# Kernel optimization log

Hardware: AMD Instinct MI355X
Metric: run time of the kernel (lower is better)

## Reference

```python
import jax, jax.numpy as jnp
import numpy as np

HID = 768
INNER = 1536   # hidden_size * expand_factor
NSTATE = 16
KCONV = 4
EPS = 1e-5


def _layernorm(x, w, b):
    mu = jnp.mean(x, axis=-1, keepdims=True)
    var = jnp.mean(jnp.square(x - mu), axis=-1, keepdims=True)
    return (x - mu) * jax.lax.rsqrt(var + EPS) * w + b


def setup_inputs() -> dict:
    key = jax.random.key(0)
    ks = jax.random.split(key, 8)
    B, S = 2, 2048
    s_in = 1.0 / np.sqrt(HID).astype(np.float32)
    s_inner = 1.0 / np.sqrt(INNER).astype(np.float32)
    s_k = 1.0 / np.sqrt(KCONV).astype(np.float32)
    return {
        "x": jax.random.normal(ks[0], (B, S, HID), jnp.float32),
        "norm_w": jnp.ones((HID,), jnp.float32),
        "norm_b": jnp.zeros((HID,), jnp.float32),
        "W_in": jax.random.normal(ks[1], (HID, 2 * INNER), jnp.float32) * s_in,
        "conv_w": jax.random.normal(ks[2], (INNER, 1, KCONV), jnp.float32) * s_k,  # OIH depthwise
        "W_xproj": jax.random.normal(ks[3], (INNER, 2 * NSTATE + INNER), jnp.float32) * s_inner,
        "A_log": jax.random.normal(ks[4], (NSTATE,), jnp.float32),
        "D": jnp.ones((INNER,), jnp.float32),
        "W_ssm_out": jax.random.normal(ks[5], (INNER, INNER), jnp.float32) * s_inner,
        "W_out": jax.random.normal(ks[6], (INNER, HID), jnp.float32) * s_inner,
    }


def _selective_ssm(u, W_xproj, A_log, D, W_ssm_out):
    # u: (B, S, INNER)
    proj = u @ W_xproj                                   # (B,S,2N+INNER)
    Bm = proj[..., :NSTATE]                              # (B,S,N)
    Cm = proj[..., NSTATE:2 * NSTATE]                    # (B,S,N)
    delta = jax.nn.softplus(proj[..., 2 * NSTATE:])      # (B,S,INNER)
    A = -jnp.exp(A_log)                                  # (N,)

    def step(h, inp):
        d_t, b_t, c_t, u_t = inp                          # (B,INNER),(B,N),(B,N),(B,INNER)
        dA = jnp.exp(d_t[:, None, :] * A[None, :, None])  # (B,N,INNER)
        h = dA * h + (d_t * u_t)[:, None, :] * b_t[:, :, None]
        y = jnp.einsum('bnh,bn->bh', h, c_t)
        return h, y

    B_, S_, _ = u.shape
    h0 = jnp.zeros((B_, NSTATE, INNER), u.dtype)
    xs = (jnp.moveaxis(delta, 1, 0), jnp.moveaxis(Bm, 1, 0),
          jnp.moveaxis(Cm, 1, 0), jnp.moveaxis(u, 1, 0))
    _, ys = jax.lax.scan(step, h0, xs)                   # (S,B,INNER)
    y = jnp.moveaxis(ys, 0, 1) + D * u
    return y @ W_ssm_out


def reference(x, norm_w, norm_b, W_in, conv_w, W_xproj, A_log, D, W_ssm_out, W_out):
    residual = x
    xn = _layernorm(x, norm_w, norm_b)
    xp = xn @ W_in                                       # (B,S,2*INNER)
    u, gate = jnp.split(xp, 2, axis=-1)
    # causal depthwise conv1d (torch pads k-1 both sides then truncates -> left pad k-1)
    uc = jax.lax.conv_general_dilated(
        jnp.swapaxes(u, 1, 2), conv_w, window_strides=(1,),
        padding=[(KCONV - 1, 0)], dimension_numbers=('NCH', 'OIH', 'NCH'),
        feature_group_count=INNER)
    u = jax.nn.silu(jnp.swapaxes(uc, 1, 2))              # (B,S,INNER)
    y = _selective_ssm(u, W_xproj, A_log, D, W_ssm_out)
    y = y * jax.nn.silu(gate)
    out = y @ W_out + residual                           # dropout is identity in eval
    return out
```

## Files before the change

### kernel.cpp

```cpp
#include <hip/hip_runtime.h>
#include <cstdint>
#include <cmath>

#define HID 768
#define INNER 1536
#define NST 16
#define SEQ 2048
#define BATCH 2
#define MTOK 4096
#define CHUNK 32
#define NCHUNK 64
#define LOG2E 1.44269504088896f

typedef unsigned short u16;
typedef __bf16 bf16x8 __attribute__((ext_vector_type(8)));
typedef float f32x4 __attribute__((ext_vector_type(4)));

__device__ __forceinline__ u16 f2b(float f) {
  union { float f; unsigned u; } a; a.f = f;
  unsigned r = a.u + 0x7FFFu + ((a.u >> 16) & 1u);
  return (u16)(r >> 16);
}
__device__ __forceinline__ float b2f(u16 h) {
  union { unsigned u; float f; } a; a.u = ((unsigned)h) << 16; return a.f;
}

__device__ __forceinline__ void gl2lds16(const u16* g, u16* l) {
  __builtin_amdgcn_global_load_lds(
      (const __attribute__((address_space(1))) void*)g,
      (__attribute__((address_space(3))) void*)l, 16, 0, 0);
}

__global__ __launch_bounds__(256)
void ln_kernel(const float* __restrict__ x, const float* __restrict__ w,
               const float* __restrict__ b, u16* __restrict__ xn) {
  const long row = blockIdx.x;
  const float* xr = x + row * HID;
  const int t = threadIdx.x;
  float v0 = xr[t], v1 = xr[t + 256], v2 = xr[t + 512];
  float s1 = v0 + v1 + v2;
  float s2 = v0 * v0 + v1 * v1 + v2 * v2;
#pragma unroll
  for (int o = 32; o > 0; o >>= 1) { s1 += __shfl_down(s1, o); s2 += __shfl_down(s2, o); }
  __shared__ float r1[4], r2[4];
  if ((t & 63) == 0) { r1[t >> 6] = s1; r2[t >> 6] = s2; }
  __syncthreads();
  s1 = r1[0] + r1[1] + r1[2] + r1[3];
  s2 = r2[0] + r2[1] + r2[2] + r2[3];
  const float mu = s1 * (1.f / HID);
  float var = s2 * (1.f / HID) - mu * mu;
  const float rs = rsqrtf(var + 1e-5f);
  xn[row * HID + t]       = f2b((v0 - mu) * rs * w[t]       + b[t]);
  xn[row * HID + t + 256] = f2b((v1 - mu) * rs * w[t + 256] + b[t + 256]);
  xn[row * HID + t + 512] = f2b((v2 - mu) * rs * w[t + 512] + b[t + 512]);
}

__global__ __launch_bounds__(256)
void transpose_cvt(const float* __restrict__ W, u16* __restrict__ Wt,
                   int K, int N, int Npad) {
  __shared__ float tb[32][33];
  const int tx = threadIdx.x, ty = threadIdx.y;
  const int n0 = blockIdx.x * 32, k0 = blockIdx.y * 32;
#pragma unroll
  for (int r = 0; r < 4; ++r) {
    int kk = k0 + ty + r * 8;
    int nn = n0 + tx;
    tb[ty + r * 8][tx] = (nn < N) ? W[(long)kk * N + nn] : 0.f;
  }
  __syncthreads();
#pragma unroll
  for (int r = 0; r < 4; ++r) {
    int nn = n0 + ty + r * 8;
    int kk = k0 + tx;
    Wt[(long)nn * K + kk] = f2b(tb[tx][ty + r * 8]);
  }
}

template <int BM, int BN, int NBX, int EPI>
__global__ __launch_bounds__(256)
void gemm_bt(const u16* __restrict__ A, const u16* __restrict__ Bt,
             float* __restrict__ O0, float* __restrict__ O1, u16* __restrict__ O2,
             const float* __restrict__ Ef, const u16* __restrict__ Eb,
             int K, int Nstore) {
  constexpr int NBY = 4096 / BM;
  constexpr int PER = NBY / 8;
  constexpr int WTM = BM / 2;
  constexpr int WTN = BN / 2;
  constexpr int FI = WTM / 16;
  constexpr int FJ = WTN / 16;
  __shared__ u16 As[BM * 32];
  __shared__ u16 Bs[BN * 32];
  const int u = blockIdx.x;
  const int xcd = u & 7;
  const int s = u >> 3;
  const int bmt = xcd * PER + s / NBX;
  const int bnt = s % NBX;
  const long bm = (long)bmt * BM;
  const long bn = (long)bnt * BN;

  const int tid = threadIdx.x;
  const int lane = tid & 63;
  const int wave = tid >> 6;
  const int wm = wave >> 1, wn = wave & 1;
  const int l16 = lane & 15, l4 = lane >> 4;

  f32x4 acc[FI][FJ] = {};

  const int r0 = tid >> 2;
  const int kg = (tid & 3) * 8;

  for (int k0 = 0; k0 < K; k0 += 32) {
#pragma unroll
    for (int q = 0; q < BM / 64; ++q)
      gl2lds16(A + (bm + r0 + q * 64) * K + kg + k0, As + ((q * 256 + tid) * 8));
#pragma unroll
    for (int q = 0; q < BN / 64; ++q)
      gl2lds16(Bt + (bn + r0 + q * 64) * K + kg + k0, Bs + ((q * 256 + tid) * 8));
    __syncthreads();
    bf16x8 af[FI], bfr[FJ];
#pragma unroll
    for (int i = 0; i < FI; ++i)
      af[i] = *(const bf16x8*)&As[(wm * WTM + i * 16 + l16) * 32 + l4 * 8];
#pragma unroll
    for (int j = 0; j < FJ; ++j)
      bfr[j] = *(const bf16x8*)&Bs[(wn * WTN + j * 16 + l16) * 32 + l4 * 8];
#pragma unroll
    for (int i = 0; i < FI; ++i)
#pragma unroll
      for (int j = 0; j < FJ; ++j)
        acc[i][j] = __builtin_amdgcn_mfma_f32_16x16x32_bf16(af[i], bfr[j], acc[i][j], 0, 0, 0);
    __syncthreads();
  }

#pragma unroll
  for (int i = 0; i < FI; ++i) {
    const long rr = bm + wm * WTM + i * 16 + l4 * 4;
#pragma unroll
    for (int j = 0; j < FJ; ++j) {
      const int cc = (int)bn + wn * WTN + j * 16 + l16;
#pragma unroll
      for (int r = 0; r < 4; ++r) {
        const long row = rr + r;
        const float v = acc[i][j][r];
        if (EPI == 0) {
          if (cc < 1536) O0[row * 1536 + cc] = v;
          else {
            float sv = v / (1.f + __expf(-v));
            O2[row * 1536 + (cc - 1536)] = f2b(sv);
          }
        } else if (EPI == 1) {
          if (cc < 16) O0[row * 16 + cc] = v;
          else if (cc < 32) O1[row * 16 + (cc - 16)] = v;
          else if (cc < Nstore) {
            float sp = (v > 20.f) ? v : log1pf(__expf(v));
            O2[row * 1536 + (cc - 32)] = f2b(sp);
          }
        } else if (EPI == 2) {
          float g = b2f(Eb[row * 1536 + cc]);
          O2[row * 1536 + cc] = f2b(v * g);
        } else {
          O0[row * 768 + cc] = v + Ef[row * 768 + cc];
        }
      }
    }
  }
}

__global__ __launch_bounds__(256)
void conv_silu(const float* __restrict__ xpu, const float* __restrict__ cw,
               u16* __restrict__ ub) {
  const int c = blockIdx.x * 256 + threadIdx.x;
  const long m = blockIdx.y;
  const int t = (int)(m & (SEQ - 1));
  const float w0 = cw[c * 4 + 0], w1 = cw[c * 4 + 1], w2 = cw[c * 4 + 2], w3 = cw[c * 4 + 3];
  float acc = w3 * xpu[m * 1536 + c];
  if (t >= 1) acc += w2 * xpu[(m - 1) * 1536 + c];
  if (t >= 2) acc += w1 * xpu[(m - 2) * 1536 + c];
  if (t >= 3) acc += w0 * xpu[(m - 3) * 1536 + c];
  const float s = acc / (1.f + __expf(-acc));
  ub[m * 1536 + c] = f2b(s);
}

__global__ __launch_bounds__(256)
void scan_phaseA(const u16* __restrict__ dlt, const u16* __restrict__ ub,
                 const float* __restrict__ Bm, const float* __restrict__ A_log,
                 float* __restrict__ P, float* __restrict__ Q) {
  const int tid = threadIdx.x;
  const int cl = tid >> 2;
  const int sg = tid & 3;
  const int c = blockIdx.x * 64 + cl;
  const int b = blockIdx.y;
  const int ch = blockIdx.z;
  float a2[4];
#pragma unroll
  for (int j = 0; j < 4; ++j) a2[j] = -__expf(A_log[sg * 4 + j]) * LOG2E;
  float h[4] = {0.f, 0.f, 0.f, 0.f};
  float sumd = 0.f;
  const long base = (long)b * SEQ + (long)ch * CHUNK;
  for (int t = 0; t < CHUNK; ++t) {
    const long m = base + t;
    const float d = b2f(dlt[m * 1536 + c]);
    const float du = d * b2f(ub[m * 1536 + c]);
    sumd += d;
    const f32x4 Bv = *(const f32x4*)&Bm[m * 16 + sg * 4];
#pragma unroll
    for (int j = 0; j < 4; ++j) {
      const float e = exp2f(a2[j] * d);
      h[j] = e * h[j] + du * Bv[j];
    }
  }
  const long sb = (((long)b * NCHUNK + ch) * NST + sg * 4) * 1536 + c;
#pragma unroll
  for (int j = 0; j < 4; ++j) {
    Q[sb + (long)j * 1536] = h[j];
    P[sb + (long)j * 1536] = exp2f(a2[j] * sumd);
  }
}

__global__ __launch_bounds__(256)
void scan_phaseB(float* __restrict__ P, const float* __restrict__ Q) {
  const long g = (long)blockIdx.x * 256 + threadIdx.x;
  const int c = (int)(g % 1536);
  const int n = (int)((g / 1536) % NST);
  const int b = (int)(g / (1536 * NST));
  float h = 0.f;
  for (int ch = 0; ch < NCHUNK; ++ch) {
    const long idx = (((long)b * NCHUNK + ch) * NST + n) * 1536 + c;
    const float p = P[idx];
    const float q = Q[idx];
    P[idx] = h;
    h = p * h + q;
  }
}

__global__ __launch_bounds__(256)
void scan_phaseC(const u16* __restrict__ dlt, const u16* __restrict__ ub,
                 const float* __restrict__ Bm, const float* __restrict__ Cm,
                 const float* __restrict__ A_log, const float* __restrict__ Dv,
                 const float* __restrict__ hs, u16* __restrict__ ys) {
  const int tid = threadIdx.x;
  const int cl = tid >> 2;
  const int sg = tid & 3;
  const int c = blockIdx.x * 64 + cl;
  const int b = blockIdx.y;
  const int ch = blockIdx.z;
  float a2[4];
#pragma unroll
  for (int j = 0; j < 4; ++j) a2[j] = -__expf(A_log[sg * 4 + j]) * LOG2E;
  float h[4];
  const long sb = (((long)b * NCHUNK + ch) * NST + sg * 4) * 1536 + c;
#pragma unroll
  for (int j = 0; j < 4; ++j) h[j] = hs[sb + (long)j * 1536];
  const float Dc = Dv[c];
  const long base = (long)b * SEQ + (long)ch * CHUNK;
  for (int t = 0; t < CHUNK; ++t) {
    const long m = base + t;
    const float d = b2f(dlt[m * 1536 + c]);
    const float uu = b2f(ub[m * 1536 + c]);
    const float du = d * uu;
    const f32x4 Bv = *(const f32x4*)&Bm[m * 16 + sg * 4];
    const f32x4 Cv = *(const f32x4*)&Cm[m * 16 + sg * 4];
    float y = (sg == 0) ? Dc * uu : 0.f;
#pragma unroll
    for (int j = 0; j < 4; ++j) {
      const float e = exp2f(a2[j] * d);
      h[j] = e * h[j] + du * Bv[j];
      y += h[j] * Cv[j];
    }
    y += __shfl_xor(y, 1);
    y += __shfl_xor(y, 2);
    if (sg == 0) ys[m * 1536 + c] = f2b(y);
  }
}

extern "C" void kernel_launch(void* const* d_in, const int* in_sizes, int n_in,
                              void* d_out, int out_size, void* d_ws, size_t ws_size,
                              hipStream_t stream) {
  const float* x     = (const float*)d_in[0];
  const float* nw    = (const float*)d_in[1];
  const float* nb    = (const float*)d_in[2];
  const float* W_in  = (const float*)d_in[3];
  const float* cw    = (const float*)d_in[4];
  const float* W_xp  = (const float*)d_in[5];
  const float* A_log = (const float*)d_in[6];
  const float* Dv    = (const float*)d_in[7];
  const float* W_so  = (const float*)d_in[8];
  const float* W_out = (const float*)d_in[9];
  float* out = (float*)d_out;

  char* w = (char*)d_ws;
  auto alloc = [&](size_t bytes) {
    char* p = w;
    w += (bytes + 255) & ~(size_t)255;
    return p;
  };
  u16*   xn    = (u16*)  alloc((size_t)MTOK * HID * 2);
  u16*   WtIn  = (u16*)  alloc((size_t)3072 * 768 * 2);
  float* xpu   = (float*)alloc((size_t)MTOK * 1536 * 4);
  u16*   sg    = (u16*)  alloc((size_t)MTOK * 1536 * 2);
  u16*   ub    = (u16*)  alloc((size_t)MTOK * 1536 * 2);
  u16*   WtXp  = (u16*)  alloc((size_t)1664 * 1536 * 2);
  float* Bmv   = (float*)alloc((size_t)MTOK * 16 * 4);
  float* Cmv   = (float*)alloc((size_t)MTOK * 16 * 4);
  u16*   dlt   = (u16*)  alloc((size_t)MTOK * 1536 * 2);
  float* P     = (float*)alloc((size_t)BATCH * NCHUNK * NST * 1536 * 4);
  float* Q     = (float*)alloc((size_t)BATCH * NCHUNK * NST * 1536 * 4);
  u16*   ys    = (u16*)  alloc((size_t)MTOK * 1536 * 2);
  u16*   WtSo  = (u16*)  alloc((size_t)1536 * 1536 * 2);
  u16*   zb    = (u16*)  alloc((size_t)MTOK * 1536 * 2);
  u16*   WtOut = (u16*)  alloc((size_t)768 * 1536 * 2);

  ln_kernel<<<MTOK, 256, 0, stream>>>(x, nw, nb, xn);
  transpose_cvt<<<dim3(3072 / 32, 768 / 32), dim3(32, 8), 0, stream>>>(W_in, WtIn, 768, 3072, 3072);
  transpose_cvt<<<dim3(1664 / 32, 1536 / 32), dim3(32, 8), 0, stream>>>(W_xp, WtXp, 1536, 1568, 1664);
  transpose_cvt<<<dim3(1536 / 32, 1536 / 32), dim3(32, 8), 0, stream>>>(W_so, WtSo, 1536, 1536, 1536);
  transpose_cvt<<<dim3(768 / 32, 1536 / 32), dim3(32, 8), 0, stream>>>(W_out, WtOut, 1536, 768, 768);

  gemm_bt<128, 128, 24, 0><<<768, 256, 0, stream>>>(xn, WtIn, xpu, nullptr, sg, nullptr, nullptr, 768, 3072);
  conv_silu<<<dim3(6, MTOK), 256, 0, stream>>>(xpu, cw, ub);
  gemm_bt<128, 64, 26, 1><<<832, 256, 0, stream>>>(ub, WtXp, Bmv, Cmv, dlt, nullptr, nullptr, 1536, 1568);
  scan_phaseA<<<dim3(24, 2, NCHUNK), 256, 0, stream>>>(dlt, ub, Bmv, A_log, P, Q);
  scan_phaseB<<<192, 256, 0, stream>>>(P, Q);
  scan_phaseC<<<dim3(24, 2, NCHUNK), 256, 0, stream>>>(dlt, ub, Bmv, Cmv, A_log, Dv, P, ys);
  gemm_bt<128, 64, 24, 2><<<768, 256, 0, stream>>>(ys, WtSo, nullptr, nullptr, zb, nullptr, sg, 1536, 1536);
  gemm_bt<64, 64, 12, 3><<<768, 256, 0, stream>>>(zb, WtOut, out, nullptr, nullptr, x, nullptr, 1536, 768);
}
```

Measured before the change: 399.1 us.

## Pack GEMM operands into MFMA fragment order and load directly to registers

Activations and weights are written in a pre-tiled layout that matches the 16x16x32 MFMA fragment order, so each lane's 8-element fragment is one contiguous 16-byte load. The GEMM drops LDS staging and both barriers per k-step and instead double-buffers fragments straight from global memory into registers. Producer kernels (layernorm, conv, scan, gating epilogue) now write the packed layout, and conv writes an extra packed copy. The trade-off is that operand tiles are no longer shared through LDS, so reuse now depends on L2, and the scattered packed-layout stores in the producers may coalesce less well.

```diff
diff --git a/kernel.cpp b/kernel.cpp
--- a/kernel.cpp
+++ b/kernel.cpp
@@ -15,6 +15,7 @@
 typedef unsigned short u16;
 typedef __bf16 bf16x8 __attribute__((ext_vector_type(8)));
 typedef float f32x4 __attribute__((ext_vector_type(4)));
+typedef u16 u16x8 __attribute__((ext_vector_type(8)));
 
 __device__ __forceinline__ u16 f2b(float f) {
   union { float f; unsigned u; } a; a.f = f;
@@ -25,15 +26,13 @@
   union { unsigned u; float f; } a; a.u = ((unsigned)h) << 16; return a.f;
 }
 
-__device__ __forceinline__ void gl2lds16(const u16* g, u16* l) {
-  __builtin_amdgcn_global_load_lds(
-      (const __attribute__((address_space(1))) void*)g,
-      (__attribute__((address_space(3))) void*)l, 16, 0, 0);
+__device__ __forceinline__ long pidx(long m, int k, int KS) {
+  return (((m >> 4) * (long)KS + (k >> 5)) * 64 + ((k >> 3) & 3) * 16 + (m & 15)) * 8 + (k & 7);
 }
 
 __global__ __launch_bounds__(256)
 void ln_kernel(const float* __restrict__ x, const float* __restrict__ w,
-               const float* __restrict__ b, u16* __restrict__ xn) {
+               const float* __restrict__ b, u16* __restrict__ xnp) {
   const long row = blockIdx.x;
   const float* xr = x + row * HID;
   const int t = threadIdx.x;
@@ -50,94 +49,96 @@
   const float mu = s1 * (1.f / HID);
   float var = s2 * (1.f / HID) - mu * mu;
   const float rs = rsqrtf(var + 1e-5f);
-  xn[row * HID + t]       = f2b((v0 - mu) * rs * w[t]       + b[t]);
-  xn[row * HID + t + 256] = f2b((v1 - mu) * rs * w[t + 256] + b[t + 256]);
-  xn[row * HID + t + 512] = f2b((v2 - mu) * rs * w[t + 512] + b[t + 512]);
-}
-
-__global__ __launch_bounds__(256)
-void transpose_cvt(const float* __restrict__ W, u16* __restrict__ Wt,
-                   int K, int N, int Npad) {
-  __shared__ float tb[32][33];
-  const int tx = threadIdx.x, ty = threadIdx.y;
-  const int n0 = blockIdx.x * 32, k0 = blockIdx.y * 32;
-#pragma unroll
-  for (int r = 0; r < 4; ++r) {
-    int kk = k0 + ty + r * 8;
-    int nn = n0 + tx;
-    tb[ty + r * 8][tx] = (nn < N) ? W[(long)kk * N + nn] : 0.f;
+  xnp[pidx(row, t,       24)] = f2b((v0 - mu) * rs * w[t]       + b[t]);
+  xnp[pidx(row, t + 256, 24)] = f2b((v1 - mu) * rs * w[t + 256] + b[t + 256]);
+  xnp[pidx(row, t + 512, 24)] = f2b((v2 - mu) * rs * w[t + 512] + b[t + 512]);
+}
+
+__global__ __launch_bounds__(256)
+void pack_w(const float* __restrict__ W, u16* __restrict__ Bp, int K, int N) {
+  __shared__ float tb[32][65];
+  const int t = threadIdx.x;
+  const int n0 = blockIdx.x * 64;
+  const int ks = blockIdx.y;
+  const int k0 = ks * 32;
+  const int KS = K >> 5;
+  {
+    const int col = t & 63, row0 = t >> 6;
+    const int nn = n0 + col;
+#pragma unroll
+    for (int rr = 0; rr < 8; ++rr) {
+      const int kk = k0 + row0 + rr * 4;
+      tb[row0 + rr * 4][col] = (nn < N) ? W[(long)kk * N + nn] : 0.f;
+    }
   }
   __syncthreads();
-#pragma unroll
-  for (int r = 0; r < 4; ++r) {
-    int nn = n0 + ty + r * 8;
-    int kk = k0 + tx;
-    Wt[(long)nn * K + kk] = f2b(tb[tx][ty + r * 8]);
-  }
-}
-
-template <int BM, int BN, int NBX, int EPI>
-__global__ __launch_bounds__(256)
-void gemm_bt(const u16* __restrict__ A, const u16* __restrict__ Bt,
+  const int ntl = t >> 6, l4 = (t >> 4) & 3, l16 = t & 15;
+  const int nl = ntl * 16 + l16;
+  u16x8 outv;
+#pragma unroll
+  for (int wdx = 0; wdx < 8; ++wdx) outv[wdx] = f2b(tb[l4 * 8 + wdx][nl]);
+  const long tile = (n0 >> 4) + ntl;
+  *(u16x8*)&Bp[(tile * KS + ks) * 512 + (l4 * 16 + l16) * 8] = outv;
+}
+
+template <int FI, int FJ, int NBLK, int EPI>
+__global__ __launch_bounds__(256)
+void gemm_pk(const u16* __restrict__ Ap, const u16* __restrict__ Bp,
              float* __restrict__ O0, float* __restrict__ O1, u16* __restrict__ O2,
              const float* __restrict__ Ef, const u16* __restrict__ Eb,
              int K, int Nstore) {
-  constexpr int NBY = 4096 / BM;
-  constexpr int PER = NBY / 8;
-  constexpr int WTM = BM / 2;
-  constexpr int WTN = BN / 2;
-  constexpr int FI = WTM / 16;
-  constexpr int FJ = WTN / 16;
-  __shared__ u16 As[BM * 32];
-  __shared__ u16 Bs[BN * 32];
+  constexpr int WM = 256 / FI;
+  constexpr int PERX = WM / 16;
+  const int KS = K >> 5;
   const int u = blockIdx.x;
+  const int wave = threadIdx.x >> 6;
+  const int lane = threadIdx.x & 63;
   const int xcd = u & 7;
   const int s = u >> 3;
-  const int bmt = xcd * PER + s / NBX;
-  const int bnt = s % NBX;
-  const long bm = (long)bmt * BM;
-  const long bn = (long)bnt * BN;
-
-  const int tid = threadIdx.x;
-  const int lane = tid & 63;
-  const int wave = tid >> 6;
-  const int wm = wave >> 1, wn = wave & 1;
+  const int wmrow = (xcd * PERX + s / NBLK) * 2 + (wave >> 1);
+  const int wn = (s % NBLK) * 2 + (wave & 1);
+
+  const u16* a0 = Ap + ((long)(wmrow * FI) * KS * 64 + lane) * 8;
+  const u16* b0 = Bp + ((long)(wn * FJ) * KS * 64 + lane) * 8;
+
+  f32x4 acc[FI][FJ] = {};
+  bf16x8 afA[FI], bfA[FJ], afB[FI], bfB[FJ];
+
+#pragma unroll
+  for (int i = 0; i < FI; ++i) afA[i] = *(const bf16x8*)(a0 + (long)i * KS * 512);
+#pragma unroll
+  for (int j = 0; j < FJ; ++j) bfA[j] = *(const bf16x8*)(b0 + (long)j * KS * 512);
+
+  for (int ks = 0; ks < KS; ks += 2) {
+#pragma unroll
+    for (int i = 0; i < FI; ++i) afB[i] = *(const bf16x8*)(a0 + ((long)i * KS + ks + 1) * 512);
+#pragma unroll
+    for (int j = 0; j < FJ; ++j) bfB[j] = *(const bf16x8*)(b0 + ((long)j * KS + ks + 1) * 512);
+#pragma unroll
+    for (int i = 0; i < FI; ++i)
+#pragma unroll
+      for (int j = 0; j < FJ; ++j)
+        acc[i][j] = __builtin_amdgcn_mfma_f32_16x16x32_bf16(afA[i], bfA[j], acc[i][j], 0, 0, 0);
+    if (ks + 2 < KS) {
+#pragma unroll
+      for (int i = 0; i < FI; ++i) afA[i] = *(const bf16x8*)(a0 + ((long)i * KS + ks + 2) * 512);
+#pragma unroll
+      for (int j = 0; j < FJ; ++j) bfA[j] = *(const bf16x8*)(b0 + ((long)j * KS + ks + 2) * 512);
+    }
+#pragma unroll
+    for (int i = 0; i < FI; ++i)
+#pragma unroll
+      for (int j = 0; j < FJ; ++j)
+        acc[i][j] = __builtin_amdgcn_mfma_f32_16x16x32_bf16(afB[i], bfB[j], acc[i][j], 0, 0, 0);
+  }
+
   const int l16 = lane & 15, l4 = lane >> 4;
-
-  f32x4 acc[FI][FJ] = {};
-
-  const int r0 = tid >> 2;
-  const int kg = (tid & 3) * 8;
-
-  for (int k0 = 0; k0 < K; k0 += 32) {
-#pragma unroll
-    for (int q = 0; q < BM / 64; ++q)
-      gl2lds16(A + (bm + r0 + q * 64) * K + kg + k0, As + ((q * 256 + tid) * 8));
-#pragma unroll
-    for (int q = 0; q < BN / 64; ++q)
-      gl2lds16(Bt + (bn + r0 + q * 64) * K + kg + k0, Bs + ((q * 256 + tid) * 8));
-    __syncthreads();
-    bf16x8 af[FI], bfr[FJ];
-#pragma unroll
-    for (int i = 0; i < FI; ++i)
-      af[i] = *(const bf16x8*)&As[(wm * WTM + i * 16 + l16) * 32 + l4 * 8];
-#pragma unroll
-    for (int j = 0; j < FJ; ++j)
-      bfr[j] = *(const bf16x8*)&Bs[(wn * WTN + j * 16 + l16) * 32 + l4 * 8];
-#pragma unroll
-    for (int i = 0; i < FI; ++i)
-#pragma unroll
-      for (int j = 0; j < FJ; ++j)
-        acc[i][j] = __builtin_amdgcn_mfma_f32_16x16x32_bf16(af[i], bfr[j], acc[i][j], 0, 0, 0);
-    __syncthreads();
-  }
-
 #pragma unroll
   for (int i = 0; i < FI; ++i) {
-    const long rr = bm + wm * WTM + i * 16 + l4 * 4;
+    const long rr = (long)(wmrow * FI + i) * 16 + l4 * 4;
 #pragma unroll
     for (int j = 0; j < FJ; ++j) {
-      const int cc = (int)bn + wn * WTN + j * 16 + l16;
+      const int cc = (wn * FJ + j) * 16 + l16;
 #pragma unroll
       for (int r = 0; r < 4; ++r) {
         const long row = rr + r;
@@ -157,7 +158,7 @@
           }
         } else if (EPI == 2) {
           float g = b2f(Eb[row * 1536 + cc]);
-          O2[row * 1536 + cc] = f2b(v * g);
+          O2[pidx(row, cc, 48)] = f2b(v * g);
         } else {
           O0[row * 768 + cc] = v + Ef[row * 768 + cc];
         }
@@ -168,7 +169,7 @@
 
 __global__ __launch_bounds__(256)
 void conv_silu(const float* __restrict__ xpu, const float* __restrict__ cw,
-               u16* __restrict__ ub) {
+               u16* __restrict__ ub, u16* __restrict__ ubp) {
   const int c = blockIdx.x * 256 + threadIdx.x;
   const long m = blockIdx.y;
   const int t = (int)(m & (SEQ - 1));
@@ -178,7 +179,9 @@
   if (t >= 2) acc += w1 * xpu[(m - 2) * 1536 + c];
   if (t >= 3) acc += w0 * xpu[(m - 3) * 1536 + c];
   const float s = acc / (1.f + __expf(-acc));
-  ub[m * 1536 + c] = f2b(s);
+  const u16 sb = f2b(s);
+  ub[m * 1536 + c] = sb;
+  ubp[pidx(m, c, 48)] = sb;
 }
 
 __global__ __launch_bounds__(256)
@@ -237,7 +240,7 @@
 void scan_phaseC(const u16* __restrict__ dlt, const u16* __restrict__ ub,
                  const float* __restrict__ Bm, const float* __restrict__ Cm,
                  const float* __restrict__ A_log, const float* __restrict__ Dv,
-                 const float* __restrict__ hs, u16* __restrict__ ys) {
+                 const float* __restrict__ hs, u16* __restrict__ ysp) {
   const int tid = threadIdx.x;
   const int cl = tid >> 2;
   const int sg = tid & 3;
@@ -269,7 +272,7 @@
     }
     y += __shfl_xor(y, 1);
     y += __shfl_xor(y, 2);
-    if (sg == 0) ys[m * 1536 + c] = f2b(y);
+    if (sg == 0) ysp[pidx(m, c, 48)] = f2b(y);
   }
 }
 
@@ -294,34 +297,35 @@
     w += (bytes + 255) & ~(size_t)255;
     return p;
   };
-  u16*   xn    = (u16*)  alloc((size_t)MTOK * HID * 2);
-  u16*   WtIn  = (u16*)  alloc((size_t)3072 * 768 * 2);
+  u16*   xnp   = (u16*)  alloc((size_t)MTOK * HID * 2);
+  u16*   WpIn  = (u16*)  alloc((size_t)3072 * 768 * 2);
   float* xpu   = (float*)alloc((size_t)MTOK * 1536 * 4);
   u16*   sg    = (u16*)  alloc((size_t)MTOK * 1536 * 2);
   u16*   ub    = (u16*)  alloc((size_t)MTOK * 1536 * 2);
-  u16*   WtXp  = (u16*)  alloc((size_t)1664 * 1536 * 2);
+  u16*   ubp   = (u16*)  alloc((size_t)MTOK * 1536 * 2);
+  u16*   WpXp  = (u16*)  alloc((size_t)1664 * 1536 * 2);
   float* Bmv   = (float*)alloc((size_t)MTOK * 16 * 4);
   float* Cmv   = (float*)alloc((size_t)MTOK * 16 * 4);
   u16*   dlt   = (u16*)  alloc((size_t)MTOK * 1536 * 2);
   float* P     = (float*)alloc((size_t)BATCH * NCHUNK * NST * 1536 * 4);
   float* Q     = (float*)alloc((size_t)BATCH * NCHUNK * NST * 1536 * 4);
-  u16*   ys    = (u16*)  alloc((size_t)MTOK * 1536 * 2);
-  u16*   WtSo  = (u16*)  alloc((size_t)1536 * 1536 * 2);
-  u16*   zb    = (u16*)  alloc((size_t)MTOK * 1536 * 2);
-  u16*   WtOut = (u16*)  alloc((size_t)768 * 1536 * 2);
-
-  ln_kernel<<<MTOK, 256, 0, stream>>>(x, nw, nb, xn);
-  transpose_cvt<<<dim3(3072 / 32, 768 / 32), dim3(32, 8), 0, stream>>>(W_in, WtIn, 768, 3072, 3072);
-  transpose_cvt<<<dim3(1664 / 32, 1536 / 32), dim3(32, 8), 0, stream>>>(W_xp, WtXp, 1536, 1568, 1664);
-  transpose_cvt<<<dim3(1536 / 32, 1536 / 32), dim3(32, 8), 0, stream>>>(W_so, WtSo, 1536, 1536, 1536);
-  transpose_cvt<<<dim3(768 / 32, 1536 / 32), dim3(32, 8), 0, stream>>>(W_out, WtOut, 1536, 768, 768);
-
-  gemm_bt<128, 128, 24, 0><<<768, 256, 0, stream>>>(xn, WtIn, xpu, nullptr, sg, nullptr, nullptr, 768, 3072);
-  conv_silu<<<dim3(6, MTOK), 256, 0, stream>>>(xpu, cw, ub);
-  gemm_bt<128, 64, 26, 1><<<832, 256, 0, stream>>>(ub, WtXp, Bmv, Cmv, dlt, nullptr, nullptr, 1536, 1568);
+  u16*   ysp   = (u16*)  alloc((size_t)MTOK * 1536 * 2);
+  u16*   WpSo  = (u16*)  alloc((size_t)1536 * 1536 * 2);
+  u16*   zbp   = (u16*)  alloc((size_t)MTOK * 1536 * 2);
+  u16*   WpOut = (u16*)  alloc((size_t)768 * 1536 * 2);
+
+  ln_kernel<<<MTOK, 256, 0, stream>>>(x, nw, nb, xnp);
+  pack_w<<<dim3(48, 24), 256, 0, stream>>>(W_in,  WpIn,  768,  3072);
+  pack_w<<<dim3(26, 48), 256, 0, stream>>>(W_xp,  WpXp,  1536, 1568);
+  pack_w<<<dim3(24, 48), 256, 0, stream>>>(W_so,  WpSo,  1536, 1536);
+  pack_w<<<dim3(12, 48), 256, 0, stream>>>(W_out, WpOut, 1536, 768);
+
+  gemm_pk<4, 4, 24, 0><<<768, 256, 0, stream>>>(xnp, WpIn, xpu, nullptr, sg, nullptr, nullptr, 768, 3072);
+  conv_silu<<<dim3(6, MTOK), 256, 0, stream>>>(xpu, cw, ub, ubp);
+  gemm_pk<4, 2, 26, 1><<<832, 256, 0, stream>>>(ubp, WpXp, Bmv, Cmv, dlt, nullptr, nullptr, 1536, 1568);
   scan_phaseA<<<dim3(24, 2, NCHUNK), 256, 0, stream>>>(dlt, ub, Bmv, A_log, P, Q);
   scan_phaseB<<<192, 256, 0, stream>>>(P, Q);
-  scan_phaseC<<<dim3(24, 2, NCHUNK), 256, 0, stream>>>(dlt, ub, Bmv, Cmv, A_log, Dv, P, ys);
-  gemm_bt<128, 64, 24, 2><<<768, 256, 0, stream>>>(ys, WtSo, nullptr, nullptr, zb, nullptr, sg, 1536, 1536);
-  gemm_bt<64, 64, 12, 3><<<768, 256, 0, stream>>>(zb, WtOut, out, nullptr, nullptr, x, nullptr, 1536, 768);
-}
+  scan_phaseC<<<dim3(24, 2, NCHUNK), 256, 0, stream>>>(dlt, ub, Bmv, Cmv, A_log, Dv, P, ysp);
+  gemm_pk<4, 2, 24, 2><<<768, 256, 0, stream>>>(ysp, WpSo, nullptr, nullptr, zbp, nullptr, sg, 1536, 1536);
+  gemm_pk<2, 2, 12, 3><<<768, 256, 0, stream>>>(zbp, WpOut, out, nullptr, nullptr, x, nullptr, 1536, 768);
+}
```

New measurement: 408.3 us. 2.3% more time.
